# Kernel tuning notes

Hardware: AMD Instinct MI355X
Metric: run time of the kernel (lower is better)

The kernel has to match this reference:

```python
import jax, jax.numpy as jnp
import numpy as np

N = 100000
E = 1600000


def _sage_conv(x, src, tgt, W_l, b, W_r):
    # PyG SAGEConv (mean aggr): out = lin_l(mean_{j in N(i)} x_j) + lin_r(x_i)
    msg = x[src]                                            # [E, F] gather
    agg = jax.ops.segment_sum(msg, tgt, num_segments=N)     # [N, F]
    deg = jax.ops.segment_sum(jnp.ones((src.shape[0],), x.dtype), tgt, num_segments=N)
    agg = agg / jnp.maximum(deg, 1.0)[:, None]               # mean
    return agg @ W_l + b + x @ W_r


def setup_inputs() -> dict:
    key = jax.random.key(0)
    ks = jax.random.split(key, 16)
    d = {
        "x": jax.random.normal(ks[0], (N, 9), jnp.float32),
        "edge_index": jax.random.randint(ks[1], (2, E), 0, N, jnp.int32).astype(jnp.int64),
        "W1_l": jax.random.normal(ks[2], (9, 128), jnp.float32) / np.sqrt(9),
        "b1": jnp.zeros((128,), jnp.float32),
        "W1_r": jax.random.normal(ks[3], (9, 128), jnp.float32) / np.sqrt(9),
        "W2_l": jax.random.normal(ks[4], (128, 128), jnp.float32) / np.sqrt(128),
        "b2": jnp.zeros((128,), jnp.float32),
        "W2_r": jax.random.normal(ks[5], (128, 128), jnp.float32) / np.sqrt(128),
        "W3_l": jax.random.normal(ks[6], (128, 128), jnp.float32) / np.sqrt(128),
        "b3": jnp.zeros((128,), jnp.float32),
        "W3_r": jax.random.normal(ks[7], (128, 128), jnp.float32) / np.sqrt(128),
        "Wl1": jax.random.normal(ks[8], (128, 128), jnp.float32) / np.sqrt(128),
        "bl1": jnp.zeros((128,), jnp.float32),
        "Wl2": jax.random.normal(ks[9], (128, 64), jnp.float32) / np.sqrt(128),
        "bl2": jnp.zeros((64,), jnp.float32),
        "Wl3": jax.random.normal(ks[10], (64, 3), jnp.float32) / np.sqrt(64),
        "bl3": jnp.zeros((3,), jnp.float32),
    }
    return d


def reference(x, edge_index, W1_l, b1, W1_r, W2_l, b2, W2_r, W3_l, b3, W3_r,
              Wl1, bl1, Wl2, bl2, Wl3, bl3):
    src, tgt = edge_index[0], edge_index[1]
    h = jax.nn.relu(_sage_conv(x, src, tgt, W1_l, b1, W1_r))   # dropout = identity (eval)
    h = jax.nn.relu(_sage_conv(h, src, tgt, W2_l, b2, W2_r))
    h = jax.nn.relu(_sage_conv(h, src, tgt, W3_l, b3, W3_r))
    h = jax.nn.relu(h @ Wl1 + bl1)
    h = jax.nn.relu(h @ Wl2 + bl2)
    h = h @ Wl3 + bl3
    return jax.nn.log_softmax(h, axis=-1)
```

## Files before the change

kernel.cpp:

```cpp
#include <hip/hip_runtime.h>
#include <hip/hip_fp16.h>
#include <stdint.h>

typedef _Float16 f16x8 __attribute__((ext_vector_type(8)));
typedef float f32x4 __attribute__((ext_vector_type(4)));


#define CH 2048
#define MAXNB 1024
#define MAXNBLK 1024

__global__ __launch_bounds__(256) void bhist_k(const int* __restrict__ ei,
        int* __restrict__ bh, int E, int shift, int NB, int NBLK) {
    __shared__ int lh[MAXNB];
    for (int b = threadIdx.x; b < NB; b += 256) lh[b] = 0;
    __syncthreads();
    int base = blockIdx.x * CH;
    int end = min(base + CH, E);
    for (int e = base + threadIdx.x; e < end; e += 256) {
        int t = ei[(size_t)E + e];
        atomicAdd(&lh[t >> shift], 1);
    }
    __syncthreads();
    for (int b = threadIdx.x; b < NB; b += 256)
        bh[(size_t)b * NBLK + blockIdx.x] = lh[b];
}

__global__ __launch_bounds__(256) void scan_col_k(int* bh, int* __restrict__ btot,
                                                  int NBLK, int NB) {
    __shared__ int sd[256];
    size_t rowoff = (size_t)blockIdx.x * NBLK;
    int t = threadIdx.x;
    int base = t * 4;
    int v0 = (base + 0 < NBLK) ? bh[rowoff + base + 0] : 0;
    int v1 = (base + 1 < NBLK) ? bh[rowoff + base + 1] : 0;
    int v2 = (base + 2 < NBLK) ? bh[rowoff + base + 2] : 0;
    int v3 = (base + 3 < NBLK) ? bh[rowoff + base + 3] : 0;
    int s = v0 + v1 + v2 + v3;
    sd[t] = s;
    __syncthreads();
    for (int off = 1; off < 256; off <<= 1) {
        int x = (t >= off) ? sd[t - off] : 0;
        __syncthreads();
        sd[t] += x;
        __syncthreads();
    }
    int ex = sd[t] - s;
    if (base + 0 < NBLK) bh[rowoff + base + 0] = ex;
    if (base + 1 < NBLK) bh[rowoff + base + 1] = ex + v0;
    if (base + 2 < NBLK) bh[rowoff + base + 2] = ex + v0 + v1;
    if (base + 3 < NBLK) bh[rowoff + base + 3] = ex + v0 + v1 + v2;
    if (t == 255) btot[blockIdx.x] = sd[255];
}

__global__ void scan_block_k(const int* __restrict__ deg, int* __restrict__ excl,
                             int* __restrict__ bsum, int N) {
    __shared__ int sd[256];
    int t = threadIdx.x;
    int base = blockIdx.x * 1024 + t * 4;
    int v0 = (base + 0 < N) ? deg[base + 0] : 0;
    int v1 = (base + 1 < N) ? deg[base + 1] : 0;
    int v2 = (base + 2 < N) ? deg[base + 2] : 0;
    int v3 = (base + 3 < N) ? deg[base + 3] : 0;
    int s = v0 + v1 + v2 + v3;
    sd[t] = s;
    __syncthreads();
    for (int off = 1; off < 256; off <<= 1) {
        int x = (t >= off) ? sd[t - off] : 0;
        __syncthreads();
        sd[t] += x;
        __syncthreads();
    }
    int incl = sd[t];
    int ex = incl - s;
    if (base + 0 < N) excl[base + 0] = ex;
    if (base + 1 < N) excl[base + 1] = ex + v0;
    if (base + 2 < N) excl[base + 2] = ex + v0 + v1;
    if (base + 3 < N) excl[base + 3] = ex + v0 + v1 + v2;
    if (t == 255) bsum[blockIdx.x] = incl;
}

__global__ __launch_bounds__(256) void bscatter_k(const int* __restrict__ ei,
        const int* __restrict__ bh, const int* __restrict__ bbase,
        int* __restrict__ staged, int E, int shift, int NB, int NBLK) {
    __shared__ int cur[MAXNB];
    for (int b = threadIdx.x; b < NB; b += 256)
        cur[b] = bbase[b] + bh[(size_t)b * NBLK + blockIdx.x];
    __syncthreads();
    int base = blockIdx.x * CH;
    int end = min(base + CH, E);
    int mask = (1 << shift) - 1;
    for (int e = base + threadIdx.x; e < end; e += 256) {
        int s = ei[e];
        int t = ei[(size_t)E + e];
        int p = atomicAdd(&cur[t >> shift], 1);
        staged[p] = s | ((t & mask) << 17);
    }
}

__global__ __launch_bounds__(256) void csrfill_k(const int* __restrict__ staged,
        const int* __restrict__ bbase, int* __restrict__ rs, int* __restrict__ csr,
        int N, int E, int shift, int NB) {
    __shared__ int lh[256];
    __shared__ int sd[256];
    int b = blockIdx.x;
    int tpb = 1 << shift;
    int t0 = b << shift;
    int s0 = bbase[b];
    int s1 = (b == NB - 1) ? E : bbase[b + 1];
    int t = threadIdx.x;
    if (t < tpb) lh[t] = 0;
    __syncthreads();
    for (int e = s0 + t; e < s1; e += 256)
        atomicAdd(&lh[staged[e] >> 17], 1);
    __syncthreads();
    int v = (t < tpb) ? lh[t] : 0;
    sd[t] = v;
    __syncthreads();
    for (int off = 1; off < 256; off <<= 1) {
        int x = (t >= off) ? sd[t - off] : 0;
        __syncthreads();
        sd[t] += x;
        __syncthreads();
    }
    if (t < tpb) {
        int excl = sd[t] - v;
        lh[t] = excl;
        int tg = t0 + t;
        if (tg < N) rs[tg] = s0 + excl;
    }
    if (b == NB - 1 && t == 0) rs[N] = E;
    __syncthreads();
    for (int e = s0 + t; e < s1; e += 256) {
        int w = staged[e];
        int lt = w >> 17;
        int src = w & 0x1FFFF;
        int p = s0 + atomicAdd(&lh[lt], 1);
        csr[p] = src;
    }
}


__global__ void agg9pack_k(const float* __restrict__ x, const int* __restrict__ rs,
                           const int* __restrict__ csr, __half* __restrict__ a32,
                           int N) {
    int i = blockIdx.x * blockDim.x + threadIdx.x;
    if (i >= N) return;
    int s0 = rs[i], s1 = rs[i + 1];
    float a[9];
    #pragma unroll
    for (int f = 0; f < 9; ++f) a[f] = 0.f;
    for (int j = s0; j < s1; ++j) {
        const float* p = x + (size_t)csr[j] * 9;
        #pragma unroll
        for (int f = 0; f < 9; ++f) a[f] += p[f];
    }
    float inv = (s1 > s0) ? 1.f / (float)(s1 - s0) : 0.f;
    const float* xr = x + (size_t)i * 9;
    union { _Float16 h[32]; uint4 u4[4]; } o;
    #pragma unroll
    for (int f = 0; f < 9; ++f) o.h[f] = (_Float16)(a[f] * inv);
    #pragma unroll
    for (int f = 0; f < 9; ++f) o.h[9 + f] = (_Float16)xr[f];
    #pragma unroll
    for (int f = 18; f < 32; ++f) o.h[f] = (_Float16)0.f;
    uint4* dst = reinterpret_cast<uint4*>(a32 + (size_t)i * 32);
    #pragma unroll
    for (int q = 0; q < 4; ++q) dst[q] = o.u4[q];
}

__global__ __launch_bounds__(256) void agg128h4_k(const __half* __restrict__ h16,
        const int* __restrict__ rs, const int* __restrict__ csr,
        __half* __restrict__ out, int N) {
    int l16 = threadIdx.x & 15;
    int node = blockIdx.x * 16 + (threadIdx.x >> 4);
    if (node >= N) return;
    int s0 = rs[node], s1 = rs[node + 1];
    const uint4* h4 = reinterpret_cast<const uint4*>(h16);
    float acc[8];
    #pragma unroll
    for (int c = 0; c < 8; ++c) acc[c] = 0.f;
    int j = s0;
    for (; j + 4 <= s1; j += 4) {
        uint4 v[4];
        #pragma unroll
        for (int u = 0; u < 4; ++u)
            v[u] = h4[(size_t)csr[j + u] * 16 + l16];
        #pragma unroll
        for (int u = 0; u < 4; ++u) {
            const __half2* p = reinterpret_cast<const __half2*>(&v[u]);
            #pragma unroll
            for (int q = 0; q < 4; ++q) {
                float2 f = __half22float2(p[q]);
                acc[q * 2]     += f.x;
                acc[q * 2 + 1] += f.y;
            }
        }
    }
    for (; j < s1; ++j) {
        uint4 vv = h4[(size_t)csr[j] * 16 + l16];
        const __half2* p = reinterpret_cast<const __half2*>(&vv);
        #pragma unroll
        for (int q = 0; q < 4; ++q) {
            float2 f = __half22float2(p[q]);
            acc[q * 2]     += f.x;
            acc[q * 2 + 1] += f.y;
        }
    }
    float inv = (s1 > s0) ? 1.f / (float)(s1 - s0) : 0.f;
    __half2 o[4];
    #pragma unroll
    for (int q = 0; q < 4; ++q)
        o[q] = __floats2half2_rn(acc[q * 2] * inv, acc[q * 2 + 1] * inv);
    reinterpret_cast<uint4*>(out)[(size_t)node * 16 + l16] =
        *reinterpret_cast<uint4*>(o);
}


struct WPD { const float* W; _Float16* dst; int K, N; };
struct WPD6 { WPD d[6]; };

__global__ void wpack6_k(WPD6 all) {
    WPD w = all.d[blockIdx.y];
    int idx = blockIdx.x * blockDim.x + threadIdx.x;
    int kcb = w.K / 32;
    int total = (w.N / 16) * kcb * 64;
    if (idx >= total) return;
    int lane = idx & 63;
    int blk = idx >> 6;
    int kb = blk % kcb;
    int nf = blk / kcb;
    int col = nf * 16 + (lane & 15);
    int k0 = kb * 32 + (lane >> 4) * 8;
    f16x8 v;
    #pragma unroll
    for (int j = 0; j < 8; ++j)
        v[j] = (_Float16)w.W[(size_t)(k0 + j) * w.N + col];
    *reinterpret_cast<f16x8*>(w.dst + (size_t)idx * 8) = v;
}

__global__ void wpack1_k(const float* __restrict__ Wl, const float* __restrict__ Wr,
                         _Float16* __restrict__ wpk) {
    int idx = blockIdx.x * blockDim.x + threadIdx.x;
    if (idx >= 8 * 64) return;
    int lane = idx & 63;
    int nf = idx >> 6;
    int col = nf * 16 + (lane & 15);
    int k0 = (lane >> 4) * 8;
    f16x8 v;
    #pragma unroll
    for (int j = 0; j < 8; ++j) {
        int k = k0 + j;
        float w = (k < 9) ? Wl[(size_t)k * 128 + col]
                : (k < 18) ? Wr[(size_t)(k - 9) * 128 + col] : 0.f;
        v[j] = (_Float16)w;
    }
    *reinterpret_cast<f16x8*>(wpk + (size_t)idx * 8) = v;
}

template<int NF, int NS, int KK>
__global__ __launch_bounds__(256) void mfma_lin_k(
        const __half* A1, const __half* A2,
        const _Float16* __restrict__ pk1, const _Float16* __restrict__ pk2,
        const float* __restrict__ bias, __half* C, int M) {
    constexpr int TN = 64 * NF;
    constexpr int KB = KK / 32;
    constexpr int LPR = KK / 8;
    constexpr int RPI = 256 / LPR;
    constexpr int ITER = 64 / RPI;
    __shared__ _Float16 a_lds[NS][64][KK + 8];

    int tid = threadIdx.x;
    int lane = tid & 63;
    int wave = tid >> 6;
    int rb = blockIdx.x * 64;

    const __half* As[2] = {A1, A2};
    #pragma unroll
    for (int s = 0; s < NS; ++s) {
        #pragma unroll
        for (int i = 0; i < ITER; ++i) {
            int row = (tid / LPR) + i * RPI;
            int c = tid % LPR;
            int grow = rb + row;
            uint4 v = make_uint4(0, 0, 0, 0);
            if (grow < M)
                v = reinterpret_cast<const uint4*>(As[s] + (size_t)grow * KK)[c];
            *reinterpret_cast<uint4*>(&a_lds[s][row][c * 8]) = v;
        }
    }

    const _Float16* pks[2] = {pk1, pk2};
    f16x8 bfrag[NS][KB][NF];
    #pragma unroll
    for (int s = 0; s < NS; ++s)
        #pragma unroll
        for (int kb = 0; kb < KB; ++kb)
            #pragma unroll
            for (int n = 0; n < NF; ++n) {
                int nf = wave * NF + n;
                bfrag[s][kb][n] =
                    reinterpret_cast<const f16x8*>(pks[s])[(size_t)(nf * KB + kb) * 64 + lane];
            }

    f32x4 acc[4][NF];
    #pragma unroll
    for (int m = 0; m < 4; ++m)
        #pragma unroll
        for (int n = 0; n < NF; ++n)
            acc[m][n] = (f32x4){0.f, 0.f, 0.f, 0.f};

    __syncthreads();

    #pragma unroll
    for (int s = 0; s < NS; ++s)
        #pragma unroll
        for (int kb = 0; kb < KB; ++kb)
            #pragma unroll
            for (int m = 0; m < 4; ++m) {
                f16x8 a = *reinterpret_cast<const f16x8*>(
                    &a_lds[s][m * 16 + (lane & 15)][kb * 32 + (lane >> 4) * 8]);
                #pragma unroll
                for (int n = 0; n < NF; ++n)
                    acc[m][n] = __builtin_amdgcn_mfma_f32_16x16x32_f16(
                        a, bfrag[s][kb][n], acc[m][n], 0, 0, 0);
            }

    #pragma unroll
    for (int n = 0; n < NF; ++n) {
        int col = wave * NF * 16 + n * 16 + (lane & 15);
        float bv = bias[col];
        #pragma unroll
        for (int m = 0; m < 4; ++m) {
            #pragma unroll
            for (int j = 0; j < 4; ++j) {
                int grow = rb + m * 16 + (lane >> 4) * 4 + j;
                if (grow < M) {
                    float v = fmaxf(acc[m][n][j] + bv, 0.f);
                    C[(size_t)grow * TN + col] = __float2half_rn(v);
                }
            }
        }
    }
}

__global__ __launch_bounds__(256) void mfma_lin_final_k(
        const __half* A1, const _Float16* __restrict__ pk1,
        const float* __restrict__ bias,
        const float* __restrict__ W3, const float* __restrict__ b3,
        float* __restrict__ outp, int M) {
    constexpr int KK = 128;
    __shared__ _Float16 a_lds[64][136];
    __shared__ float smem[64][68];

    int tid = threadIdx.x;
    int lane = tid & 63;
    int wave = tid >> 6;
    int rb = blockIdx.x * 64;

    #pragma unroll
    for (int i = 0; i < 4; ++i) {
        int row = (tid >> 4) + i * 16;
        int grow = rb + row;
        uint4 v = make_uint4(0, 0, 0, 0);
        if (grow < M)
            v = reinterpret_cast<const uint4*>(A1 + (size_t)grow * KK)[tid & 15];
        *reinterpret_cast<uint4*>(&a_lds[row][(tid & 15) * 8]) = v;
    }

    f16x8 bfrag[4];
    #pragma unroll
    for (int kb = 0; kb < 4; ++kb)
        bfrag[kb] = reinterpret_cast<const f16x8*>(pk1)[(size_t)(wave * 4 + kb) * 64 + lane];

    f32x4 acc[4];
    #pragma unroll
    for (int m = 0; m < 4; ++m) acc[m] = (f32x4){0.f, 0.f, 0.f, 0.f};

    __syncthreads();

    #pragma unroll
    for (int kb = 0; kb < 4; ++kb)
        #pragma unroll
        for (int m = 0; m < 4; ++m) {
            f16x8 a = *reinterpret_cast<const f16x8*>(
                &a_lds[m * 16 + (lane & 15)][kb * 32 + (lane >> 4) * 8]);
            acc[m] = __builtin_amdgcn_mfma_f32_16x16x32_f16(a, bfrag[kb], acc[m], 0, 0, 0);
        }

    int col = wave * 16 + (lane & 15);
    float bv = bias[col];
    #pragma unroll
    for (int m = 0; m < 4; ++m)
        #pragma unroll
        for (int j = 0; j < 4; ++j) {
            int row = m * 16 + (lane >> 4) * 4 + j;
            smem[row][col] = fmaxf(acc[m][j] + bv, 0.f);
        }
    __syncthreads();

    if (tid < 64) {
        int grow = rb + tid;
        if (grow < M) {
            float l0 = b3[0], l1 = b3[1], l2 = b3[2];
            #pragma unroll 8
            for (int k = 0; k < 64; ++k) {
                float v = smem[tid][k];
                l0 = fmaf(v, W3[k * 3 + 0], l0);
                l1 = fmaf(v, W3[k * 3 + 1], l1);
                l2 = fmaf(v, W3[k * 3 + 2], l2);
            }
            float mx = fmaxf(l0, fmaxf(l1, l2));
            float e0 = expf(l0 - mx), e1 = expf(l1 - mx), e2 = expf(l2 - mx);
            float lse = logf(e0 + e1 + e2) + mx;
            outp[(size_t)grow * 3 + 0] = l0 - lse;
            outp[(size_t)grow * 3 + 1] = l1 - lse;
            outp[(size_t)grow * 3 + 2] = l2 - lse;
        }
    }
}


extern "C" void kernel_launch(void* const* d_in, const int* in_sizes, int n_in,
                              void* d_out, int out_size, void* d_ws, size_t ws_size,
                              hipStream_t stream) {
    const float* x   = (const float*)d_in[0];
    const int* ei    = (const int*)d_in[1];
    const float* W1l = (const float*)d_in[2];
    const float* b1  = (const float*)d_in[3];
    const float* W1r = (const float*)d_in[4];
    const float* W2l = (const float*)d_in[5];
    const float* b2  = (const float*)d_in[6];
    const float* W2r = (const float*)d_in[7];
    const float* W3l = (const float*)d_in[8];
    const float* b3  = (const float*)d_in[9];
    const float* W3r = (const float*)d_in[10];
    const float* Wl1 = (const float*)d_in[11];
    const float* bl1 = (const float*)d_in[12];
    const float* Wl2 = (const float*)d_in[13];
    const float* bl2 = (const float*)d_in[14];
    const float* Wl3 = (const float*)d_in[15];
    const float* bl3 = (const float*)d_in[16];
    float* out = (float*)d_out;

    const int N = in_sizes[0] / 9;
    const int E = in_sizes[1] / 2;

    char* ws = (char*)d_ws;
    size_t off = 0;
    auto alloc = [&](size_t bytes) -> void* {
        void* p = ws + off;
        off += (bytes + 255) & ~(size_t)255;
        return p;
    };
    __half* h16    = (__half*)alloc((size_t)N * 128 * sizeof(__half));
    __half* agg16  = (__half*)alloc((size_t)N * 128 * sizeof(__half));
    __half* a32    = (__half*)alloc((size_t)N * 32 * sizeof(__half));
    int* rs     = (int*)alloc((size_t)(N + 1) * sizeof(int));
    int* csr    = (int*)alloc((size_t)E * sizeof(int));
    int* staged = (int*)alloc((size_t)E * sizeof(int));
    _Float16* wpk1  = (_Float16*)alloc(32 * 128 * sizeof(_Float16));
    _Float16* wpk2l = (_Float16*)alloc(128 * 128 * sizeof(_Float16));
    _Float16* wpk2r = (_Float16*)alloc(128 * 128 * sizeof(_Float16));
    _Float16* wpk3l = (_Float16*)alloc(128 * 128 * sizeof(_Float16));
    _Float16* wpk3r = (_Float16*)alloc(128 * 128 * sizeof(_Float16));
    _Float16* wpkl1 = (_Float16*)alloc(128 * 128 * sizeof(_Float16));
    _Float16* wpkl2 = (_Float16*)alloc(128 * 64 * sizeof(_Float16));
    (void)ws_size; (void)n_in; (void)out_size;

    int shift = 7;
    while ((((size_t)N + ((size_t)1 << shift) - 1) >> shift) > MAXNB) ++shift;
    const int NB = (N + (1 << shift) - 1) >> shift;
    const int NBLK = (E + CH - 1) / CH;
    int* bh    = (int*)alloc((size_t)NB * NBLK * sizeof(int));
    int* btot  = (int*)alloc((size_t)NB * sizeof(int));
    int* bbase = (int*)alloc((size_t)(NB + 1) * sizeof(int));
    int* bsum  = (int*)alloc(64 * sizeof(int));

    WPD6 wp;
    wp.d[0] = {W2l, wpk2l, 128, 128};
    wp.d[1] = {W2r, wpk2r, 128, 128};
    wp.d[2] = {W3l, wpk3l, 128, 128};
    wp.d[3] = {W3r, wpk3r, 128, 128};
    wp.d[4] = {Wl1, wpkl1, 128, 128};
    wp.d[5] = {Wl2, wpkl2, 128, 64};
    wpack6_k<<<dim3(8, 6), 256, 0, stream>>>(wp);
    wpack1_k<<<2, 256, 0, stream>>>(W1l, W1r, wpk1);

    bhist_k<<<NBLK, 256, 0, stream>>>(ei, bh, E, shift, NB, NBLK);
    scan_col_k<<<NB, 256, 0, stream>>>(bh, btot, NBLK, NB);
    scan_block_k<<<1, 256, 0, stream>>>(btot, bbase, bsum, NB);
    bscatter_k<<<NBLK, 256, 0, stream>>>(ei, bh, bbase, staged, E, shift, NB, NBLK);
    csrfill_k<<<NB, 256, 0, stream>>>(staged, bbase, rs, csr, N, E, shift, NB);

    const int gemm_grid = (N + 63) / 64;
    const int agg_grid = (N + 15) / 16;

    agg9pack_k<<<(N + 255) / 256, 256, 0, stream>>>(x, rs, csr, a32, N);
    mfma_lin_k<2, 1, 32><<<gemm_grid, 256, 0, stream>>>(
        a32, nullptr, wpk1, nullptr, b1, h16, N);

    agg128h4_k<<<agg_grid, 256, 0, stream>>>(h16, rs, csr, agg16, N);
    mfma_lin_k<2, 2, 128><<<gemm_grid, 256, 0, stream>>>(
        agg16, h16, wpk2l, wpk2r, b2, h16, N);

    agg128h4_k<<<agg_grid, 256, 0, stream>>>(h16, rs, csr, agg16, N);
    mfma_lin_k<2, 2, 128><<<gemm_grid, 256, 0, stream>>>(
        agg16, h16, wpk3l, wpk3r, b3, h16, N);

    mfma_lin_k<2, 1, 128><<<gemm_grid, 256, 0, stream>>>(
        h16, nullptr, wpkl1, nullptr, bl1, h16, N);
    mfma_lin_final_k<<<gemm_grid, 256, 0, stream>>>(
        h16, wpkl2, bl2, Wl3, bl3, out, N);
}
```

Baseline: 294.8 us.

## Gather layer-1 features from packed fp16 copy and coarsen CSR build chunks

Adds a pre-pass that casts the 9-wide fp32 node features into a 32-byte-aligned fp16 row, so the layer-1 neighbor gather does one 16-byte plus one 4-byte load per edge instead of nine scalar fp32 loads. The gather loop is unrolled by two to keep more loads in flight. Separately, the CSR-build chunk size grows from 2048 to 16384 edges and the starting bucket shift from 7 to 8, giving fewer histogram/scatter blocks and fewer buckets. This costs an extra kernel launch and buffer, rounds the neighbor inputs to fp16 before averaging, and leaves fewer blocks to parallelise the CSR build.

```diff
diff --git a/kernel.cpp b/kernel.cpp
--- a/kernel.cpp
+++ b/kernel.cpp
@@ -6,9 +6,8 @@
 typedef float f32x4 __attribute__((ext_vector_type(4)));
 
 
-#define CH 2048
+#define CH 16384
 #define MAXNB 1024
-#define MAXNBLK 1024
 
 __global__ __launch_bounds__(256) void bhist_k(const int* __restrict__ ei,
         int* __restrict__ bh, int E, int shift, int NB, int NBLK) {
@@ -141,27 +140,55 @@
 }
 
 
-__global__ void agg9pack_k(const float* __restrict__ x, const int* __restrict__ rs,
+__global__ void xcast_k(const float* __restrict__ x, __half* __restrict__ x16,
+                        int N) {
+    int i = blockIdx.x * blockDim.x + threadIdx.x;
+    if (i >= N) return;
+    const float* xr = x + (size_t)i * 9;
+    union { _Float16 h[16]; uint4 u4[2]; } o;
+    #pragma unroll
+    for (int f = 0; f < 9; ++f) o.h[f] = (_Float16)xr[f];
+    #pragma unroll
+    for (int f = 9; f < 16; ++f) o.h[f] = (_Float16)0.f;
+    uint4* dst = reinterpret_cast<uint4*>(x16 + (size_t)i * 16);
+    dst[0] = o.u4[0];
+    dst[1] = o.u4[1];
+}
+
+__global__ void agg9pack_k(const __half* __restrict__ x16, const int* __restrict__ rs,
                            const int* __restrict__ csr, __half* __restrict__ a32,
                            int N) {
     int i = blockIdx.x * blockDim.x + threadIdx.x;
     if (i >= N) return;
     int s0 = rs[i], s1 = rs[i + 1];
+    const uint4* h4 = reinterpret_cast<const uint4*>(x16);
     float a[9];
     #pragma unroll
     for (int f = 0; f < 9; ++f) a[f] = 0.f;
-    for (int j = s0; j < s1; ++j) {
-        const float* p = x + (size_t)csr[j] * 9;
-        #pragma unroll
-        for (int f = 0; f < 9; ++f) a[f] += p[f];
-    }
+    auto acc9 = [&](int src) {
+        uint4 va = h4[(size_t)src * 2];
+        unsigned int wb = *reinterpret_cast<const unsigned int*>(
+            x16 + (size_t)src * 16 + 8);
+        const __half2* p = reinterpret_cast<const __half2*>(&va);
+        #pragma unroll
+        for (int q = 0; q < 4; ++q) {
+            float2 f = __half22float2(p[q]);
+            a[q * 2]     += f.x;
+            a[q * 2 + 1] += f.y;
+        }
+        __half2 h8 = *reinterpret_cast<const __half2*>(&wb);
+        a[8] += __half22float2(h8).x;
+    };
+    int j = s0;
+    for (; j + 2 <= s1; j += 2) { acc9(csr[j]); acc9(csr[j + 1]); }
+    if (j < s1) acc9(csr[j]);
     float inv = (s1 > s0) ? 1.f / (float)(s1 - s0) : 0.f;
-    const float* xr = x + (size_t)i * 9;
     union { _Float16 h[32]; uint4 u4[4]; } o;
     #pragma unroll
     for (int f = 0; f < 9; ++f) o.h[f] = (_Float16)(a[f] * inv);
-    #pragma unroll
-    for (int f = 0; f < 9; ++f) o.h[9 + f] = (_Float16)xr[f];
+    const _Float16* sx = reinterpret_cast<const _Float16*>(x16 + (size_t)i * 16);
+    #pragma unroll
+    for (int f = 0; f < 9; ++f) o.h[9 + f] = sx[f];
     #pragma unroll
     for (int f = 18; f < 32; ++f) o.h[f] = (_Float16)0.f;
     uint4* dst = reinterpret_cast<uint4*>(a32 + (size_t)i * 32);
@@ -456,6 +483,7 @@
     __half* h16    = (__half*)alloc((size_t)N * 128 * sizeof(__half));
     __half* agg16  = (__half*)alloc((size_t)N * 128 * sizeof(__half));
     __half* a32    = (__half*)alloc((size_t)N * 32 * sizeof(__half));
+    __half* x16    = (__half*)alloc((size_t)N * 16 * sizeof(__half));
     int* rs     = (int*)alloc((size_t)(N + 1) * sizeof(int));
     int* csr    = (int*)alloc((size_t)E * sizeof(int));
     int* staged = (int*)alloc((size_t)E * sizeof(int));
@@ -468,7 +496,7 @@
     _Float16* wpkl2 = (_Float16*)alloc(128 * 64 * sizeof(_Float16));
     (void)ws_size; (void)n_in; (void)out_size;
 
-    int shift = 7;
+    int shift = 8;
     while ((((size_t)N + ((size_t)1 << shift) - 1) >> shift) > MAXNB) ++shift;
     const int NB = (N + (1 << shift) - 1) >> shift;
     const int NBLK = (E + CH - 1) / CH;
@@ -486,6 +514,7 @@
     wp.d[5] = {Wl2, wpkl2, 128, 64};
     wpack6_k<<<dim3(8, 6), 256, 0, stream>>>(wp);
     wpack1_k<<<2, 256, 0, stream>>>(W1l, W1r, wpk1);
+    xcast_k<<<(N + 255) / 256, 256, 0, stream>>>(x, x16, N);
 
     bhist_k<<<NBLK, 256, 0, stream>>>(ei, bh, E, shift, NB, NBLK);
     scan_col_k<<<NB, 256, 0, stream>>>(bh, btot, NBLK, NB);
@@ -496,7 +525,7 @@
     const int gemm_grid = (N + 63) / 64;
     const int agg_grid = (N + 15) / 16;
 
-    agg9pack_k<<<(N + 255) / 256, 256, 0, stream>>>(x, rs, csr, a32, N);
+    agg9pack_k<<<(N + 255) / 256, 256, 0, stream>>>(x16, rs, csr, a32, N);
     mfma_lin_k<2, 1, 32><<<gemm_grid, 256, 0, stream>>>(
         a32, nullptr, wpk1, nullptr, b1, h16, N);
 
```

Result: slower. 303.4 us, median of 2 (+2.9%).
